# Kernel optimization log

Measured on AMD Instinct MI355X. Metric: run time of the kernel, lower is better.

Reference implementation:

```python
import jax, jax.numpy as jnp
import numpy as np

N = 768  # length of time vector

def setup_inputs() -> dict:
    key = jax.random.key(0)
    ks = jax.random.split(key, 4)
    # time vector (sorted grid-like values, as in a GP time axis)
    x = jnp.sort(jax.random.uniform(ks[0], (N,), dtype=jnp.float32) * (6 * np.pi))
    # MLP params: Linear(2,1024) -> Sigmoid -> Linear(1024,128) -> ReLU -> Linear(128,1)
    W1 = jax.random.normal(ks[1], (1024, 2), dtype=jnp.float32) * (1.0 / np.sqrt(2.0))
    b1 = jnp.zeros((1024,), dtype=jnp.float32)
    W2 = jax.random.normal(ks[2], (128, 1024), dtype=jnp.float32) * (1.0 / np.sqrt(1024.0))
    b2 = jnp.zeros((128,), dtype=jnp.float32)
    W3 = jax.random.normal(ks[3], (1, 128), dtype=jnp.float32) * (1.0 / np.sqrt(128.0))
    b3 = jnp.zeros((1,), dtype=jnp.float32)
    return {"x": x, "W1": W1, "b1": b1, "W2": W2, "b2": b2, "W3": W3, "b3": b3}


def reference(x, W1, b1, W2, b2, W3, b3):
    n = x.shape[0]
    # all (i, j) with j >= i  -> n(n+1)/2 pairs; replaces the Python double loop
    iu, ju = jnp.triu_indices(n)
    pairs = jnp.stack([x[iu], x[ju]], axis=-1)            # [P, 2]
    h = jax.nn.sigmoid(pairs @ W1.T + b1)                 # [P, 1024]
    h = jax.nn.relu(h @ W2.T + b2)                        # [P, 128]
    v = (h @ W3.T + b3)[:, 0]                             # [P]
    # K starts as eye; upper triangle INCLUDING diagonal is overwritten
    K = jnp.eye(n, dtype=x.dtype).at[iu, ju].set(v)       # [n, n] upper-triangular
    return K.T @ K                                        # symmetric PSD covariance
```

## Files before the change

kernel.cpp:

```cpp
#include <hip/hip_runtime.h>
#include <hip/hip_bf16.h>

#define NN 768
#define MD 1024
#define NPAIR 295296
#define NPBLK2 2307

typedef __attribute__((ext_vector_type(8))) short s16x8;
typedef __attribute__((ext_vector_type(4))) float f32x4;
typedef __attribute__((ext_vector_type(2))) float f32x2;
typedef __attribute__((ext_vector_type(2))) __bf16 b16x2;

__device__ __forceinline__ ushort bf16_rn(float f) {
    uint u = __builtin_bit_cast(uint, f);
    u += 0x7FFFu + ((u >> 16) & 1u);
    return (ushort)(u >> 16);
}

__device__ __forceinline__ void ptoij(int p, int& io, int& jo) {
    const float disc = (float)(1537 * 1537 - 8 * p);
    int i = (int)((1537.0f - sqrtf(disc)) * 0.5f);
    i = i < 0 ? 0 : (i > 767 ? 767 : i);
    while (i > 0 && p < i * (1537 - i) / 2) --i;
    while (i < 767 && p >= (i + 1) * (1536 - i) / 2) ++i;
    io = i;
    jo = i + (p - i * (1537 - i) / 2);
}

#define GLOAD16(gsrc, ldst)                                                        \
    __builtin_amdgcn_global_load_lds(                                              \
        (const __attribute__((address_space(1))) void*)(gsrc),                     \
        (__attribute__((address_space(3))) void*)(ldst), 16, 0, 0)

__global__ __launch_bounds__(256) void w2frag(const float* __restrict__ W2,
                                              ushort* __restrict__ WF)
{
    const int id = blockIdx.x * 256 + threadIdx.x;
    const int lane = id & 63;
    const int f = id >> 6;
    const int tn = f & 7;
    const int ks = (f >> 3) & 1;
    const int c  = f >> 4;
    const int k = tn * 16 + (lane & 15);
    const int m = c * 64 + ks * 32 + (lane >> 4) * 8;
    const float4 a = *reinterpret_cast<const float4*>(W2 + k * MD + m);
    const float4 b = *reinterpret_cast<const float4*>(W2 + k * MD + m + 4);
    const float w[8] = {a.x, a.y, a.z, a.w, b.x, b.y, b.z, b.w};
    s16x8 h;
#pragma unroll
    for (int e = 0; e < 8; ++e) h[e] = (short)bf16_rn(w[e]);
    *reinterpret_cast<s16x8*>(WF + id * 8) = h;
}

__global__ __launch_bounds__(256) void eaprep(const float* __restrict__ x,
                                              const float* __restrict__ W1,
                                              const float* __restrict__ b1,
                                              float* __restrict__ EAg)
{
    const int i = blockIdx.x;
    const float xi = x[i];
    const float NL2E = -1.4426950408889634f;
    for (int m = threadIdx.x; m < MD; m += 256) {
        const float2 w = reinterpret_cast<const float2*>(W1)[m];
        EAg[i * MD + m] = __builtin_amdgcn_exp2f(fmaf(w.x, xi, b1[m]) * NL2E);
    }
}

__global__ __launch_bounds__(256) void ecfprep(const float* __restrict__ x,
                                               const float* __restrict__ W1,
                                               ushort* __restrict__ ECF)
{
    const int id = blockIdx.x * 256 + threadIdx.x;
    const int j = id >> 7;
    const int m8 = id & 127;
    const float xj = x[j];
    const float NL2E = -1.4426950408889634f;
    const int mbase = m8 * 8;
    s16x8 h;
#pragma unroll
    for (int e = 0; e < 8; ++e) {
        const float cm = W1[(mbase + e) * 2 + 1];
        h[e] = (short)bf16_rn(__builtin_amdgcn_exp2f(cm * xj * NL2E));
    }
    const int c    = mbase >> 6;
    const int ks   = (mbase >> 5) & 1;
    const int l4   = (mbase & 31) >> 3;
    const int lane = l4 * 16 + (j & 15);
    const int off  = (j >> 4) * 16384 + c * 1024 + ks * 512 + lane * 8;
    *reinterpret_cast<s16x8*>(ECF + off) = h;
}

#define LOADB_T(cc, ks)                                                      \
    {                                                                        \
        const ushort* wb_ = WF + (cc) * 8192 + (ks) * 4096 + lane * 8;       \
        _Pragma("unroll")                                                    \
        for (int tn_ = 0; tn_ < 8; ++tn_)                                    \
            bh[tn_] = *reinterpret_cast<const s16x8*>(wb_ + tn_ * 512);      \
    }

#define LOADEC(cc, ks, dst)                                                  \
    {                                                                        \
        const ushort* e_ = ECF + jg0 * 16384 + (cc) * 1024 + (ks) * 512 + lane * 8; \
        dst[0] = *reinterpret_cast<const s16x8*>(e_);                        \
        dst[1] = *reinterpret_cast<const s16x8*>(e_ + 16384);                \
    }

#define SIG_T(cc, ks_, ec)                                                   \
    {                                                                        \
        const int m0_ = (cc) * 64 + (ks_) * 32 + l4 * 8;                     \
        const f32x4 ea0_ = *reinterpret_cast<const f32x4*>(&EAl[m0_]);       \
        const f32x4 ea1_ = *reinterpret_cast<const f32x4*>(&EAl[m0_ + 4]);   \
        _Pragma("unroll")                                                    \
        for (int tm_ = 0; tm_ < 2; ++tm_) {                                  \
            union { s16x8 v; uint u[4]; } ec_;                               \
            ec_.v = ec[tm_];                                                 \
            union { s16x8 v; uint u[4]; } fr_;                               \
            _Pragma("unroll")                                                \
            for (int h_ = 0; h_ < 4; ++h_) {                                 \
                const uint uu_ = ec_.u[h_];                                  \
                const float el_ = __builtin_bit_cast(float, uu_ << 16);      \
                const float eh_ = __builtin_bit_cast(float, uu_ & 0xFFFF0000u); \
                const float ga_ = (h_ < 2) ? ea0_[2 * h_] : ea1_[2 * h_ - 4];     \
                const float gb_ = (h_ < 2) ? ea0_[2 * h_ + 1] : ea1_[2 * h_ - 3]; \
                const float t0_ = fmaf(el_, ga_, 1.0f);                      \
                const float t1_ = fmaf(eh_, gb_, 1.0f);                      \
                b16x2 p_;                                                    \
                p_.x = (__bf16)__builtin_amdgcn_rcpf(t0_);                   \
                p_.y = (__bf16)__builtin_amdgcn_rcpf(t1_);                   \
                fr_.u[h_] = __builtin_bit_cast(uint, p_);                    \
            }                                                                \
            ah[tm_] = fr_.v;                                                 \
        }                                                                    \
    }

#define MFMA_T()                                                             \
    {                                                                        \
        __builtin_amdgcn_s_setprio(1);                                       \
        _Pragma("unroll")                                                    \
        for (int tm_ = 0; tm_ < 2; ++tm_)                                    \
            _Pragma("unroll")                                                \
            for (int tn_ = 0; tn_ < 8; ++tn_)                                \
                acc[tm_][tn_] = __builtin_amdgcn_mfma_f32_16x16x32_bf16(     \
                    ah[tm_], bh[tn_], acc[tm_][tn_], 0, 0, 0);               \
        __builtin_amdgcn_s_setprio(0);                                       \
    }

__global__ __launch_bounds__(256, 3) void mlp_tab(
    const float* __restrict__ EAg, const ushort* __restrict__ ECF,
    const ushort* __restrict__ WF,
    const float* __restrict__ b2, const float* __restrict__ W3,
    const float* __restrict__ b3, float* __restrict__ K)
{
    const int i  = blockIdx.y;
    const int j0 = blockIdx.x * 128;
    if (j0 + 127 < i) return;

    __shared__ __align__(16) float EAl[MD];

    const int t = threadIdx.x;
    const int lane = t & 63, wv = t >> 6;
    const int l15 = lane & 15, l4 = lane >> 4;

    const int jw  = j0 + wv * 32;
    const int jg0 = jw >> 4;

    GLOAD16(EAg + i * MD + wv * 256 + lane * 4, (char*)EAl + wv * 1024);

    f32x4 acc[2][8];
#pragma unroll
    for (int a = 0; a < 2; ++a)
#pragma unroll
        for (int b = 0; b < 8; ++b) acc[a][b] = (f32x4){0.f, 0.f, 0.f, 0.f};

    s16x8 bh[8], ecA[2], ecB[2], ah[2];
    LOADB_T(0, 0);
    LOADEC(0, 0, ecA);
    __syncthreads();

    for (int c = 0; c < 16; ++c) {
        LOADEC(c, 1, ecB);
        SIG_T(c, 0, ecA);
        MFMA_T();
        LOADB_T(c, 1);
        if (c < 15) LOADEC(c + 1, 0, ecA);
        SIG_T(c, 1, ecB);
        MFMA_T();
        if (c < 15) LOADB_T(c + 1, 0);
    }

    float w3v[8], b2v[8];
#pragma unroll
    for (int tn = 0; tn < 8; ++tn) {
        const int k = tn * 16 + l15;
        w3v[tn] = W3[k];
        b2v[tn] = b2[k];
    }
    const float b3v = b3[0];
#pragma unroll
    for (int tm = 0; tm < 2; ++tm)
#pragma unroll
        for (int r = 0; r < 4; ++r) {
            float v = 0.f;
#pragma unroll
            for (int tn = 0; tn < 8; ++tn)
                v = fmaf(w3v[tn], fmaxf(acc[tm][tn][r] + b2v[tn], 0.f), v);
            v += __shfl_xor(v, 1, 16);
            v += __shfl_xor(v, 2, 16);
            v += __shfl_xor(v, 4, 16);
            v += __shfl_xor(v, 8, 16);
            if (l15 == 0) {
                const int j = jw + tm * 16 + l4 * 4 + r;
                if (j >= i) K[i * NN + j] = v + b3v;
            }
        }
}

#define LOADB(cc, ks)                                                        \
    {                                                                        \
        const ushort* wb_ = WF + (cc) * 8192 + (ks) * 4096 + lane * 8;       \
        _Pragma("unroll")                                                    \
        for (int tn_ = 0; tn_ < 8; ++tn_)                                    \
            bh[tn_] = *reinterpret_cast<const s16x8*>(wb_ + tn_ * 512);      \
    }

#define SIG_HALF(cc, ks_)                                                    \
    {                                                                        \
        const int m0_ = (cc) * 64 + (ks_) * 32 + l4 * 8;                     \
        const f32x4 a0_ = *reinterpret_cast<const f32x4*>(&sa[m0_]);         \
        const f32x4 a1_ = *reinterpret_cast<const f32x4*>(&sa[m0_ + 4]);     \
        const f32x4 c0_ = *reinterpret_cast<const f32x4*>(&sc[m0_]);         \
        const f32x4 c1_ = *reinterpret_cast<const f32x4*>(&sc[m0_ + 4]);     \
        const f32x4 b0_ = *reinterpret_cast<const f32x4*>(&sb[m0_]);         \
        const f32x4 b1_ = *reinterpret_cast<const f32x4*>(&sb[m0_ + 4]);     \
        _Pragma("unroll")                                                    \
        for (int tm_ = 0; tm_ < 2; ++tm_) {                                  \
            const f32x2 xi2_ = (f32x2){xia[tm_], xia[tm_]};                  \
            const f32x2 xj2_ = (f32x2){xja[tm_], xja[tm_]};                  \
            const f32x2 one2_ = (f32x2){1.f, 1.f};                           \
            union { s16x8 v; uint u[4]; } fr_;                               \
            _Pragma("unroll")                                                \
            for (int h_ = 0; h_ < 4; ++h_) {                                 \
                f32x2 av_, cv_, bv_;                                         \
                if (h_ < 2) {                                                \
                    av_ = (f32x2){a0_[2 * h_], a0_[2 * h_ + 1]};             \
                    cv_ = (f32x2){c0_[2 * h_], c0_[2 * h_ + 1]};             \
                    bv_ = (f32x2){b0_[2 * h_], b0_[2 * h_ + 1]};             \
                } else {                                                     \
                    av_ = (f32x2){a1_[2 * h_ - 4], a1_[2 * h_ - 3]};         \
                    cv_ = (f32x2){c1_[2 * h_ - 4], c1_[2 * h_ - 3]};         \
                    bv_ = (f32x2){b1_[2 * h_ - 4], b1_[2 * h_ - 3]};         \
                }                                                            \
                const f32x2 u2_ = __builtin_elementwise_fma(                 \
                    xi2_, av_, __builtin_elementwise_fma(xj2_, cv_, bv_));   \
                f32x2 e2_;                                                   \
                e2_[0] = __builtin_amdgcn_exp2f(u2_[0]);                     \
                e2_[1] = __builtin_amdgcn_exp2f(u2_[1]);                     \
                const f32x2 t2_ = e2_ + one2_;                               \
                b16x2 p_;                                                    \
                p_.x = (__bf16)__builtin_amdgcn_rcpf(t2_[0]);                \
                p_.y = (__bf16)__builtin_amdgcn_rcpf(t2_[1]);                \
                fr_.u[h_] = __builtin_bit_cast(uint, p_);                    \
            }                                                                \
            ah[tm_] = fr_.v;                                                 \
        }                                                                    \
    }

#define MFMA_HALF()                                                          \
    {                                                                        \
        __builtin_amdgcn_s_setprio(1);                                       \
        _Pragma("unroll")                                                    \
        for (int tm_ = 0; tm_ < 2; ++tm_)                                    \
            _Pragma("unroll")                                                \
            for (int tn_ = 0; tn_ < 8; ++tn_)                                \
                acc[tm_][tn_] = __builtin_amdgcn_mfma_f32_16x16x32_bf16(     \
                    ah[tm_], bh[tn_], acc[tm_][tn_], 0, 0, 0);               \
        __builtin_amdgcn_s_setprio(0);                                       \
    }

__global__ __launch_bounds__(256, 3) void mlp_pairs_reg(
    const float* __restrict__ x,
    const float* __restrict__ W1, const float* __restrict__ b1,
    const ushort* __restrict__ WF,
    const float* __restrict__ b2, const float* __restrict__ W3,
    const float* __restrict__ b3, float* __restrict__ K)
{
    __shared__ __align__(16) float sa[MD], sc[MD], sb[MD];

    const int t = threadIdx.x;
    const int lane = t & 63;
    const int l15 = lane & 15, l4 = lane >> 4;
    const int wv = t >> 6;

    const float NL2E = -1.4426950408889634f;
    for (int m = t; m < MD; m += 256) {
        const float2 w = reinterpret_cast<const float2*>(W1)[m];
        sa[m] = w.x * NL2E;
        sc[m] = w.y * NL2E;
        sb[m] = b1[m] * NL2E;
    }

    const int pairbase = blockIdx.x * 128 + wv * 32;

    float xia[2], xja[2];
#pragma unroll
    for (int tm = 0; tm < 2; ++tm) {
        const int p = pairbase + tm * 16 + l15;
        if (p < NPAIR) {
            int i, j;
            ptoij(p, i, j);
            xia[tm] = x[i];
            xja[tm] = x[j];
        } else {
            xia[tm] = 0.f;
            xja[tm] = 0.f;
        }
    }

    f32x4 acc[2][8];
#pragma unroll
    for (int a = 0; a < 2; ++a)
#pragma unroll
        for (int b = 0; b < 8; ++b) acc[a][b] = (f32x4){0.f, 0.f, 0.f, 0.f};

    s16x8 bh[8];
    LOADB(0, 0);
    __syncthreads();

    s16x8 ah[2];
    for (int c = 0; c < 16; ++c) {
        SIG_HALF(c, 0);
        MFMA_HALF();
        LOADB(c, 1);
        SIG_HALF(c, 1);
        MFMA_HALF();
        if (c < 15) LOADB(c + 1, 0);
    }

    float w3v[8], b2v[8];
#pragma unroll
    for (int tn = 0; tn < 8; ++tn) {
        const int k = tn * 16 + l15;
        w3v[tn] = W3[k];
        b2v[tn] = b2[k];
    }
    const float b3v = b3[0];
#pragma unroll
    for (int tm = 0; tm < 2; ++tm)
#pragma unroll
        for (int r = 0; r < 4; ++r) {
            float v = 0.f;
#pragma unroll
            for (int tn = 0; tn < 8; ++tn)
                v = fmaf(w3v[tn], fmaxf(acc[tm][tn][r] + b2v[tn], 0.f), v);
            v += __shfl_xor(v, 1, 16);
            v += __shfl_xor(v, 2, 16);
            v += __shfl_xor(v, 4, 16);
            v += __shfl_xor(v, 8, 16);
            if (l15 == 0) {
                const int p = pairbase + tm * 16 + l4 * 4 + r;
                if (p < NPAIR) {
                    int i, j;
                    ptoij(p, i, j);
                    K[i * NN + j] = v + b3v;
                }
            }
        }
}

__global__ __launch_bounds__(256) void ktk(const float* __restrict__ K,
                                           float* __restrict__ C)
{
    const int b0 = blockIdx.x * 64;
    const int a0 = blockIdx.y * 64;
    if (b0 < a0) return;
    __shared__ float Ka[64][68];
    __shared__ float Kb[64][68];
    const int t  = threadIdx.x;
    const int tb = t & 15;
    const int ta = t >> 4;
    float acc[4][4];
#pragma unroll
    for (int u = 0; u < 4; u++)
#pragma unroll
        for (int v = 0; v < 4; v++) acc[u][v] = 0.f;
    const int kmax = a0 + 64;
    for (int k0 = 0; k0 < kmax; k0 += 64) {
#pragma unroll
        for (int q = 0; q < 4; q++) {
            const int f  = t + q * 256;
            const int kk = f >> 4;
            const int c4 = (f & 15) * 4;
            *reinterpret_cast<float4*>(&Ka[kk][c4]) =
                *reinterpret_cast<const float4*>(K + (k0 + kk) * NN + a0 + c4);
            *reinterpret_cast<float4*>(&Kb[kk][c4]) =
                *reinterpret_cast<const float4*>(K + (k0 + kk) * NN + b0 + c4);
        }
        __syncthreads();
#pragma unroll 8
        for (int kk = 0; kk < 64; kk++) {
            const float4 av = *reinterpret_cast<const float4*>(&Ka[kk][ta * 4]);
            const float4 bv = *reinterpret_cast<const float4*>(&Kb[kk][tb * 4]);
            const float a4[4] = {av.x, av.y, av.z, av.w};
            const float b4[4] = {bv.x, bv.y, bv.z, bv.w};
#pragma unroll
            for (int u = 0; u < 4; u++)
#pragma unroll
                for (int v = 0; v < 4; v++)
                    acc[u][v] = fmaf(a4[u], b4[v], acc[u][v]);
        }
        __syncthreads();
    }
#pragma unroll
    for (int u = 0; u < 4; u++) {
        float4 o;
        o.x = acc[u][0]; o.y = acc[u][1]; o.z = acc[u][2]; o.w = acc[u][3];
        *reinterpret_cast<float4*>(C + (a0 + ta * 4 + u) * NN + b0 + tb * 4) = o;
    }
    if (b0 > a0) {
#pragma unroll
        for (int v = 0; v < 4; v++) {
            float4 o;
            o.x = acc[0][v]; o.y = acc[1][v]; o.z = acc[2][v]; o.w = acc[3][v];
            *reinterpret_cast<float4*>(C + (b0 + tb * 4 + v) * NN + a0 + ta * 4) = o;
        }
    }
}

extern "C" void kernel_launch(void* const* d_in, const int* in_sizes, int n_in,
                              void* d_out, int out_size, void* d_ws, size_t ws_size,
                              hipStream_t stream)
{
    const float* x  = (const float*)d_in[0];
    const float* W1 = (const float*)d_in[1];
    const float* b1 = (const float*)d_in[2];
    const float* W2 = (const float*)d_in[3];
    const float* b2 = (const float*)d_in[4];
    const float* W3 = (const float*)d_in[5];
    const float* b3 = (const float*)d_in[6];
    float* Kmat = (float*)d_ws;
    float* C    = (float*)d_out;

    const size_t kBytes  = (size_t)NN * NN * sizeof(float);
    const size_t wBytes  = 262144;
    const size_t eaB     = (size_t)NN * MD * sizeof(float);
    const size_t ecB     = (size_t)48 * 16384 * sizeof(ushort);
    const size_t needTab = kBytes + wBytes + eaB + ecB;
    const size_t needFB  = kBytes + wBytes;

    hipMemsetAsync(Kmat, 0, kBytes, stream);
    if (ws_size >= needTab) {
        ushort* WF  = (ushort*)((char*)d_ws + kBytes);
        float*  EAg = (float*)((char*)d_ws + kBytes + wBytes);
        ushort* ECF = (ushort*)((char*)d_ws + kBytes + wBytes + eaB);
        w2frag<<<64, 256, 0, stream>>>(W2, WF);
        eaprep<<<NN, 256, 0, stream>>>(x, W1, b1, EAg);
        ecfprep<<<384, 256, 0, stream>>>(x, W1, ECF);
        mlp_tab<<<dim3(6, NN), 256, 0, stream>>>(EAg, ECF, WF, b2, W3, b3, Kmat);
    } else if (ws_size >= needFB) {
        ushort* WF = (ushort*)((char*)d_ws + kBytes);
        w2frag<<<64, 256, 0, stream>>>(W2, WF);
        mlp_pairs_reg<<<NPBLK2, 256, 0, stream>>>(x, W1, b1, WF, b2, W3, b3, Kmat);
    }
    ktk<<<dim3(NN / 64, NN / 64), 256, 0, stream>>>(Kmat, C);
}
```

Before: 179.9 us.

## Schedule MLP by compact triangular strip table and fuse prep kernels

The MLP kernel's 2D grid of (i, 128-column chunk) blocks is replaced by a compact table listing only the 16-column strips that touch the upper triangle. Each wave handles two such strips, which may come from different rows i. This cuts the wasted MFMA work on strips lying entirely below the diagonal and evens out the load across blocks. EA is now read straight from global memory rather than staged in LDS, and the three prep kernels plus the new table build are merged into one launch to save launch overhead. The trade-offs are an extra indirection through the table and the loss of LDS sharing of EA.

New measurement: 186.1 us. 1.03x slower.

```diff
diff --git a/kernel.cpp b/kernel.cpp
--- a/kernel.cpp
+++ b/kernel.cpp
@@ -5,6 +5,8 @@
 #define MD 1024
 #define NPAIR 295296
 #define NPBLK2 2307
+#define NSTRIP 18816
+#define NSBLK 2352
 
 typedef __attribute__((ext_vector_type(8))) short s16x8;
 typedef __attribute__((ext_vector_type(4))) float f32x4;
@@ -27,10 +29,196 @@
     jo = i + (p - i * (1537 - i) / 2);
 }
 
-#define GLOAD16(gsrc, ldst)                                                        \
-    __builtin_amdgcn_global_load_lds(                                              \
-        (const __attribute__((address_space(1))) void*)(gsrc),                     \
-        (__attribute__((address_space(3))) void*)(ldst), 16, 0, 0)
+__global__ __launch_bounds__(256) void prep_all(
+    const float* __restrict__ x,  const float* __restrict__ W1,
+    const float* __restrict__ b1, const float* __restrict__ W2,
+    ushort* __restrict__ WF, ushort* __restrict__ ECF,
+    int* __restrict__ stab, float* __restrict__ EAg)
+{
+    const int b = blockIdx.x;
+    const float NL2E = -1.4426950408889634f;
+    if (b < 64) {
+        const int id = b * 256 + threadIdx.x;
+        const int lane = id & 63;
+        const int f = id >> 6;
+        const int tn = f & 7;
+        const int ks = (f >> 3) & 1;
+        const int c  = f >> 4;
+        const int k = tn * 16 + (lane & 15);
+        const int m = c * 64 + ks * 32 + (lane >> 4) * 8;
+        const float4 a = *reinterpret_cast<const float4*>(W2 + k * MD + m);
+        const float4 bb = *reinterpret_cast<const float4*>(W2 + k * MD + m + 4);
+        const float w[8] = {a.x, a.y, a.z, a.w, bb.x, bb.y, bb.z, bb.w};
+        s16x8 h;
+#pragma unroll
+        for (int e = 0; e < 8; ++e) h[e] = (short)bf16_rn(w[e]);
+        *reinterpret_cast<s16x8*>(WF + id * 8) = h;
+    } else if (b < 448) {
+        const int id = (b - 64) * 256 + threadIdx.x;
+        const int j = id >> 7;
+        const int m8 = id & 127;
+        const float xj = x[j];
+        const int mbase = m8 * 8;
+        s16x8 h;
+#pragma unroll
+        for (int e = 0; e < 8; ++e) {
+            const float cm = W1[(mbase + e) * 2 + 1];
+            h[e] = (short)bf16_rn(__builtin_amdgcn_exp2f(cm * xj * NL2E));
+        }
+        const int c    = mbase >> 6;
+        const int ks   = (mbase >> 5) & 1;
+        const int l4   = (mbase & 31) >> 3;
+        const int lane = l4 * 16 + (j & 15);
+        const int off  = (j >> 4) * 16384 + c * 1024 + ks * 512 + lane * 8;
+        *reinterpret_cast<s16x8*>(ECF + off) = h;
+    } else if (b < 592) {
+        const int id = (b - 448) * 256 + threadIdx.x;
+        if (id < 768 * 48) {
+            const int i = id / 48;
+            const int q = id - i * 48;
+            const int g = i >> 4;
+            if (q >= g) {
+                const int slot = 8 * g * (97 - g) + (i & 15) * (48 - g) + (q - g);
+                stab[slot] = (i << 6) | q;
+            }
+        }
+    } else {
+        const int id = (b - 592) * 256 + threadIdx.x;
+        const int i = id >> 10;
+        const int m = id & 1023;
+        const float2 w = reinterpret_cast<const float2*>(W1)[m];
+        EAg[id] = __builtin_amdgcn_exp2f(fmaf(w.x, x[i], b1[m]) * NL2E);
+    }
+}
+
+#define LOADB_T(cc, ks)                                                      \
+    {                                                                        \
+        const ushort* wb_ = WF + (cc) * 8192 + (ks) * 4096 + lane * 8;       \
+        _Pragma("unroll")                                                    \
+        for (int tn_ = 0; tn_ < 8; ++tn_)                                    \
+            bh[tn_] = *reinterpret_cast<const s16x8*>(wb_ + tn_ * 512);      \
+    }
+
+#define LOADEC_S(cc, ks, dst)                                                \
+    {                                                                        \
+        const int o_ = (cc) * 1024 + (ks) * 512 + lane * 8;                  \
+        dst[0] = *reinterpret_cast<const s16x8*>(ec0base + o_);              \
+        dst[1] = *reinterpret_cast<const s16x8*>(ec1base + o_);              \
+    }
+
+#define SIG_ONE(eabase, ecv, dst_ah)                                         \
+    {                                                                        \
+        const f32x4 ea0_ = *reinterpret_cast<const f32x4*>(eabase + m0_);    \
+        const f32x4 ea1_ = *reinterpret_cast<const f32x4*>(eabase + m0_ + 4);\
+        union { s16x8 v; uint u[4]; } ec_;                                   \
+        ec_.v = ecv;                                                         \
+        union { s16x8 v; uint u[4]; } fr_;                                   \
+        _Pragma("unroll")                                                    \
+        for (int h_ = 0; h_ < 4; ++h_) {                                     \
+            const uint uu_ = ec_.u[h_];                                      \
+            const float el_ = __builtin_bit_cast(float, uu_ << 16);          \
+            const float eh_ = __builtin_bit_cast(float, uu_ & 0xFFFF0000u);  \
+            const float ga_ = (h_ < 2) ? ea0_[2 * h_] : ea1_[2 * h_ - 4];    \
+            const float gb_ = (h_ < 2) ? ea0_[2 * h_ + 1] : ea1_[2 * h_ - 3];\
+            const float t0_ = fmaf(el_, ga_, 1.0f);                          \
+            const float t1_ = fmaf(eh_, gb_, 1.0f);                          \
+            b16x2 p_;                                                        \
+            p_.x = (__bf16)__builtin_amdgcn_rcpf(t0_);                       \
+            p_.y = (__bf16)__builtin_amdgcn_rcpf(t1_);                       \
+            fr_.u[h_] = __builtin_bit_cast(uint, p_);                        \
+        }                                                                    \
+        dst_ah = fr_.v;                                                      \
+    }
+
+#define SIG_S(cc, ks_, ec)                                                   \
+    {                                                                        \
+        const int m0_ = (cc) * 64 + (ks_) * 32 + l4 * 8;                     \
+        SIG_ONE(ea0base, ec[0], ah[0]);                                      \
+        SIG_ONE(ea1base, ec[1], ah[1]);                                      \
+    }
+
+#define MFMA_T()                                                             \
+    {                                                                        \
+        __builtin_amdgcn_s_setprio(1);                                       \
+        _Pragma("unroll")                                                    \
+        for (int tm_ = 0; tm_ < 2; ++tm_)                                    \
+            _Pragma("unroll")                                                \
+            for (int tn_ = 0; tn_ < 8; ++tn_)                                \
+                acc[tm_][tn_] = __builtin_amdgcn_mfma_f32_16x16x32_bf16(     \
+                    ah[tm_], bh[tn_], acc[tm_][tn_], 0, 0, 0);               \
+        __builtin_amdgcn_s_setprio(0);                                       \
+    }
+
+__global__ __launch_bounds__(256, 3) void mlp_strip(
+    const float* __restrict__ EAg, const ushort* __restrict__ ECF,
+    const ushort* __restrict__ WF, const int* __restrict__ stab,
+    const float* __restrict__ b2, const float* __restrict__ W3,
+    const float* __restrict__ b3, float* __restrict__ K)
+{
+    const int t = threadIdx.x;
+    const int lane = t & 63, wv = t >> 6;
+    const int l15 = lane & 15, l4 = lane >> 4;
+
+    const int gw = blockIdx.x * 4 + wv;
+    const int s0 = stab[2 * gw], s1 = stab[2 * gw + 1];
+    const int i0_ = s0 >> 6, jg0_ = s0 & 63;
+    const int i1_ = s1 >> 6, jg1_ = s1 & 63;
+
+    const float* ea0base = EAg + i0_ * MD;
+    const float* ea1base = EAg + i1_ * MD;
+    const ushort* ec0base = ECF + jg0_ * 16384;
+    const ushort* ec1base = ECF + jg1_ * 16384;
+
+    f32x4 acc[2][8];
+#pragma unroll
+    for (int a = 0; a < 2; ++a)
+#pragma unroll
+        for (int b = 0; b < 8; ++b) acc[a][b] = (f32x4){0.f, 0.f, 0.f, 0.f};
+
+    s16x8 bh[8], ecA[2], ecB[2], ah[2];
+    LOADB_T(0, 0);
+    LOADEC_S(0, 0, ecA);
+
+    for (int c = 0; c < 16; ++c) {
+        LOADEC_S(c, 1, ecB);
+        SIG_S(c, 0, ecA);
+        MFMA_T();
+        LOADB_T(c, 1);
+        if (c < 15) LOADEC_S(c + 1, 0, ecA);
+        SIG_S(c, 1, ecB);
+        MFMA_T();
+        if (c < 15) LOADB_T(c + 1, 0);
+    }
+
+    float w3v[8], b2v[8];
+#pragma unroll
+    for (int tn = 0; tn < 8; ++tn) {
+        const int k = tn * 16 + l15;
+        w3v[tn] = W3[k];
+        b2v[tn] = b2[k];
+    }
+    const float b3v = b3[0];
+#pragma unroll
+    for (int tm = 0; tm < 2; ++tm) {
+        const int iS  = (tm == 0) ? i0_ : i1_;
+        const int jgS = (tm == 0) ? jg0_ : jg1_;
+#pragma unroll
+        for (int r = 0; r < 4; ++r) {
+            float v = 0.f;
+#pragma unroll
+            for (int tn = 0; tn < 8; ++tn)
+                v = fmaf(w3v[tn], fmaxf(acc[tm][tn][r] + b2v[tn], 0.f), v);
+            v += __shfl_xor(v, 1, 16);
+            v += __shfl_xor(v, 2, 16);
+            v += __shfl_xor(v, 4, 16);
+            v += __shfl_xor(v, 8, 16);
+            if (l15 == 0) {
+                const int j = jgS * 16 + l4 * 4 + r;
+                if (j >= iS) K[iS * NN + j] = v + b3v;
+            }
+        }
+    }
+}
 
 __global__ __launch_bounds__(256) void w2frag(const float* __restrict__ W2,
                                               ushort* __restrict__ WF)
@@ -50,169 +238,6 @@
 #pragma unroll
     for (int e = 0; e < 8; ++e) h[e] = (short)bf16_rn(w[e]);
     *reinterpret_cast<s16x8*>(WF + id * 8) = h;
-}
-
-__global__ __launch_bounds__(256) void eaprep(const float* __restrict__ x,
-                                              const float* __restrict__ W1,
-                                              const float* __restrict__ b1,
-                                              float* __restrict__ EAg)
-{
-    const int i = blockIdx.x;
-    const float xi = x[i];
-    const float NL2E = -1.4426950408889634f;
-    for (int m = threadIdx.x; m < MD; m += 256) {
-        const float2 w = reinterpret_cast<const float2*>(W1)[m];
-        EAg[i * MD + m] = __builtin_amdgcn_exp2f(fmaf(w.x, xi, b1[m]) * NL2E);
-    }
-}
-
-__global__ __launch_bounds__(256) void ecfprep(const float* __restrict__ x,
-                                               const float* __restrict__ W1,
-                                               ushort* __restrict__ ECF)
-{
-    const int id = blockIdx.x * 256 + threadIdx.x;
-    const int j = id >> 7;
-    const int m8 = id & 127;
-    const float xj = x[j];
-    const float NL2E = -1.4426950408889634f;
-    const int mbase = m8 * 8;
-    s16x8 h;
-#pragma unroll
-    for (int e = 0; e < 8; ++e) {
-        const float cm = W1[(mbase + e) * 2 + 1];
-        h[e] = (short)bf16_rn(__builtin_amdgcn_exp2f(cm * xj * NL2E));
-    }
-    const int c    = mbase >> 6;
-    const int ks   = (mbase >> 5) & 1;
-    const int l4   = (mbase & 31) >> 3;
-    const int lane = l4 * 16 + (j & 15);
-    const int off  = (j >> 4) * 16384 + c * 1024 + ks * 512 + lane * 8;
-    *reinterpret_cast<s16x8*>(ECF + off) = h;
-}
-
-#define LOADB_T(cc, ks)                                                      \
-    {                                                                        \
-        const ushort* wb_ = WF + (cc) * 8192 + (ks) * 4096 + lane * 8;       \
-        _Pragma("unroll")                                                    \
-        for (int tn_ = 0; tn_ < 8; ++tn_)                                    \
-            bh[tn_] = *reinterpret_cast<const s16x8*>(wb_ + tn_ * 512);      \
-    }
-
-#define LOADEC(cc, ks, dst)                                                  \
-    {                                                                        \
-        const ushort* e_ = ECF + jg0 * 16384 + (cc) * 1024 + (ks) * 512 + lane * 8; \
-        dst[0] = *reinterpret_cast<const s16x8*>(e_);                        \
-        dst[1] = *reinterpret_cast<const s16x8*>(e_ + 16384);                \
-    }
-
-#define SIG_T(cc, ks_, ec)                                                   \
-    {                                                                        \
-        const int m0_ = (cc) * 64 + (ks_) * 32 + l4 * 8;                     \
-        const f32x4 ea0_ = *reinterpret_cast<const f32x4*>(&EAl[m0_]);       \
-        const f32x4 ea1_ = *reinterpret_cast<const f32x4*>(&EAl[m0_ + 4]);   \
-        _Pragma("unroll")                                                    \
-        for (int tm_ = 0; tm_ < 2; ++tm_) {                                  \
-            union { s16x8 v; uint u[4]; } ec_;                               \
-            ec_.v = ec[tm_];                                                 \
-            union { s16x8 v; uint u[4]; } fr_;                               \
-            _Pragma("unroll")                                                \
-            for (int h_ = 0; h_ < 4; ++h_) {                                 \
-                const uint uu_ = ec_.u[h_];                                  \
-                const float el_ = __builtin_bit_cast(float, uu_ << 16);      \
-                const float eh_ = __builtin_bit_cast(float, uu_ & 0xFFFF0000u); \
-                const float ga_ = (h_ < 2) ? ea0_[2 * h_] : ea1_[2 * h_ - 4];     \
-                const float gb_ = (h_ < 2) ? ea0_[2 * h_ + 1] : ea1_[2 * h_ - 3]; \
-                const float t0_ = fmaf(el_, ga_, 1.0f);                      \
-                const float t1_ = fmaf(eh_, gb_, 1.0f);                      \
-                b16x2 p_;                                                    \
-                p_.x = (__bf16)__builtin_amdgcn_rcpf(t0_);                   \
-                p_.y = (__bf16)__builtin_amdgcn_rcpf(t1_);                   \
-                fr_.u[h_] = __builtin_bit_cast(uint, p_);                    \
-            }                                                                \
-            ah[tm_] = fr_.v;                                                 \
-        }                                                                    \
-    }
-
-#define MFMA_T()                                                             \
-    {                                                                        \
-        __builtin_amdgcn_s_setprio(1);                                       \
-        _Pragma("unroll")                                                    \
-        for (int tm_ = 0; tm_ < 2; ++tm_)                                    \
-            _Pragma("unroll")                                                \
-            for (int tn_ = 0; tn_ < 8; ++tn_)                                \
-                acc[tm_][tn_] = __builtin_amdgcn_mfma_f32_16x16x32_bf16(     \
-                    ah[tm_], bh[tn_], acc[tm_][tn_], 0, 0, 0);               \
-        __builtin_amdgcn_s_setprio(0);                                       \
-    }
-
-__global__ __launch_bounds__(256, 3) void mlp_tab(
-    const float* __restrict__ EAg, const ushort* __restrict__ ECF,
-    const ushort* __restrict__ WF,
-    const float* __restrict__ b2, const float* __restrict__ W3,
-    const float* __restrict__ b3, float* __restrict__ K)
-{
-    const int i  = blockIdx.y;
-    const int j0 = blockIdx.x * 128;
-    if (j0 + 127 < i) return;
-
-    __shared__ __align__(16) float EAl[MD];
-
-    const int t = threadIdx.x;
-    const int lane = t & 63, wv = t >> 6;
-    const int l15 = lane & 15, l4 = lane >> 4;
-
-    const int jw  = j0 + wv * 32;
-    const int jg0 = jw >> 4;
-
-    GLOAD16(EAg + i * MD + wv * 256 + lane * 4, (char*)EAl + wv * 1024);
-
-    f32x4 acc[2][8];
-#pragma unroll
-    for (int a = 0; a < 2; ++a)
-#pragma unroll
-        for (int b = 0; b < 8; ++b) acc[a][b] = (f32x4){0.f, 0.f, 0.f, 0.f};
-
-    s16x8 bh[8], ecA[2], ecB[2], ah[2];
-    LOADB_T(0, 0);
-    LOADEC(0, 0, ecA);
-    __syncthreads();
-
-    for (int c = 0; c < 16; ++c) {
-        LOADEC(c, 1, ecB);
-        SIG_T(c, 0, ecA);
-        MFMA_T();
-        LOADB_T(c, 1);
-        if (c < 15) LOADEC(c + 1, 0, ecA);
-        SIG_T(c, 1, ecB);
-        MFMA_T();
-        if (c < 15) LOADB_T(c + 1, 0);
-    }
-
-    float w3v[8], b2v[8];
-#pragma unroll
-    for (int tn = 0; tn < 8; ++tn) {
-        const int k = tn * 16 + l15;
-        w3v[tn] = W3[k];
-        b2v[tn] = b2[k];
-    }
-    const float b3v = b3[0];
-#pragma unroll
-    for (int tm = 0; tm < 2; ++tm)
-#pragma unroll
-        for (int r = 0; r < 4; ++r) {
-            float v = 0.f;
-#pragma unroll
-            for (int tn = 0; tn < 8; ++tn)
-                v = fmaf(w3v[tn], fmaxf(acc[tm][tn][r] + b2v[tn], 0.f), v);
-            v += __shfl_xor(v, 1, 16);
-            v += __shfl_xor(v, 2, 16);
-            v += __shfl_xor(v, 4, 16);
-            v += __shfl_xor(v, 8, 16);
-            if (l15 == 0) {
-                const int j = jw + tm * 16 + l4 * 4 + r;
-                if (j >= i) K[i * NN + j] = v + b3v;
-            }
-        }
 }
 
 #define LOADB(cc, ks)                                                        \
@@ -444,7 +469,8 @@
     const size_t wBytes  = 262144;
     const size_t eaB     = (size_t)NN * MD * sizeof(float);
     const size_t ecB     = (size_t)48 * 16384 * sizeof(ushort);
-    const size_t needTab = kBytes + wBytes + eaB + ecB;
+    const size_t stB     = (size_t)NSTRIP * sizeof(int);
+    const size_t needTab = kBytes + wBytes + eaB + ecB + stB;
     const size_t needFB  = kBytes + wBytes;
 
     hipMemsetAsync(Kmat, 0, kBytes, stream);
@@ -452,10 +478,9 @@
         ushort* WF  = (ushort*)((char*)d_ws + kBytes);
         float*  EAg = (float*)((char*)d_ws + kBytes + wBytes);
         ushort* ECF = (ushort*)((char*)d_ws + kBytes + wBytes + eaB);
-        w2frag<<<64, 256, 0, stream>>>(W2, WF);
-        eaprep<<<NN, 256, 0, stream>>>(x, W1, b1, EAg);
-        ecfprep<<<384, 256, 0, stream>>>(x, W1, ECF);
-        mlp_tab<<<dim3(6, NN), 256, 0, stream>>>(EAg, ECF, WF, b2, W3, b3, Kmat);
+        int*    stab = (int*)((char*)d_ws + kBytes + wBytes + eaB + ecB);
+        prep_all<<<3664, 256, 0, stream>>>(x, W1, b1, W2, WF, ECF, stab, EAg);
+        mlp_strip<<<NSBLK, 256, 0, stream>>>(EAg, ECF, WF, stab, b2, W3, b3, Kmat);
     } else if (ws_size >= needFB) {
         ushort* WF = (ushort*)((char*)d_ws + kBytes);
         w2frag<<<64, 256, 0, stream>>>(W2, WF);
```
